# Optimization experiments

Measured on AMD Instinct MI355X. Metric: run time of the kernel, lower is better.

## Reference

```python
import jax, jax.numpy as jnp
import numpy as np

NUM_GROUPS = 32
NUM_HEADS = 8
EPS = 1e-5


def setup_inputs() -> dict:
    key = jax.random.key(0)
    ks = jax.random.split(key, 4)
    b, c, h, w = 16, 512, 32, 32
    x = jax.random.normal(ks[0], (b, c, h, w), dtype=jnp.float32)
    norm_w = jnp.ones((c,), dtype=jnp.float32)
    norm_b = jnp.zeros((c,), dtype=jnp.float32)
    qkv_w = jax.random.normal(ks[1], (3 * c, c), dtype=jnp.float32) * (1.0 / np.sqrt(c))
    qkv_b = jnp.zeros((3 * c,), dtype=jnp.float32)
    proj_w = jax.random.normal(ks[2], (c, c), dtype=jnp.float32) * (1.0 / np.sqrt(c))
    proj_b = jnp.zeros((c,), dtype=jnp.float32)
    return {"x": x, "norm_w": norm_w, "norm_b": norm_b,
            "qkv_w": qkv_w, "qkv_b": qkv_b, "proj_w": proj_w, "proj_b": proj_b}


def group_norm(x, weight, bias):
    b, c, h, w = x.shape
    xg = x.reshape(b, NUM_GROUPS, c // NUM_GROUPS, h * w)
    mean = xg.mean(axis=(2, 3), keepdims=True)
    var = xg.var(axis=(2, 3), keepdims=True)
    xn = (xg - mean) * jax.lax.rsqrt(var + EPS)
    xn = xn.reshape(b, c, h, w)
    return xn * weight[None, :, None, None] + bias[None, :, None, None]


def reference(x, norm_w, norm_b, qkv_w, qkv_b, proj_w, proj_b):
    b, c, h, w = x.shape
    n = h * w
    head = NUM_HEADS
    ch = c // head

    x_norm = group_norm(x, norm_w, norm_b)
    # 1x1 conv == channel matmul: [b,3c,n]
    xf = x_norm.reshape(b, c, n)
    qkv = jnp.einsum('oc,bcn->bon', qkv_w, xf) + qkv_b[None, :, None]
    q, k, v = jnp.split(qkv, 3, axis=1)  # each [b,c,n]
    q = q.reshape(b, head, ch, n) * (ch ** -0.5)
    k = k.reshape(b, head, ch, n)
    v = v.reshape(b, head, ch, n)

    attn = jnp.einsum('bhcn,bhcm->bhnm', q, k)
    attn = jax.nn.softmax(attn, axis=-1)
    out = jnp.einsum('bhnm,bhcm->bhcn', attn, v)  # [b,head,ch,n]
    out = out.reshape(b, c, n)
    out = jnp.einsum('oc,bcn->bon', proj_w, out) + proj_b[None, :, None]
    return x + out.reshape(b, c, h, w)
```

## Files before the change

### kernel.cpp

```cpp
#include <hip/hip_runtime.h>

typedef short short8 __attribute__((ext_vector_type(8)));
typedef short short4v __attribute__((ext_vector_type(4)));
typedef float f32x4 __attribute__((ext_vector_type(4)));

#define B_   16
#define C_   512
#define N_   1024
#define NH_  8
#define CH_  64
#define G_   32
#define CPG_ 16

#if __has_builtin(__builtin_amdgcn_mfma_f32_16x16x16bf16_1k)
#define HAVE_M16 1
#endif

__device__ inline float b2f(unsigned int u) {
    union { unsigned int i; float f; } v; v.i = u << 16; return v.f;
}
__device__ inline unsigned short f2b(float f) {
    union { float f; unsigned int i; } v; v.f = f;
    unsigned int r = v.i + 0x7fffu + ((v.i >> 16) & 1u);
    return (unsigned short)(r >> 16);
}
__device__ inline unsigned int pack2(float a, float b) {
    return (unsigned int)f2b(a) | ((unsigned int)f2b(b) << 16);
}
__device__ inline unsigned int asu(float f) {
    union { float f; unsigned int i; } v; v.f = f; return v.i;
}
__device__ inline unsigned int packtr(float a, float b) {
    return __builtin_amdgcn_perm(asu(b), asu(a), 0x07060302u);
}
__device__ inline void gload16(const void* g, void* l) {
    __builtin_amdgcn_global_load_lds(
        (const __attribute__((address_space(1))) void*)g,
        (__attribute__((address_space(3))) void*)l, 16, 0, 0);
}

__global__ __launch_bounds__(256) void gnconv_kernel(const float* __restrict__ x,
                                                     const float* __restrict__ nw,
                                                     const float* __restrict__ nb,
                                                     unsigned short* __restrict__ xnT,
                                                     const float* __restrict__ qkvw,
                                                     const float* __restrict__ projw,
                                                     unsigned short* __restrict__ wq,
                                                     unsigned short* __restrict__ wp)
{
    __shared__ float red[8];
    int t = threadIdx.x;

    if (blockIdx.x >= 512) {
        const int NQ = 3 * C_ * C_;
        int idx = (((int)blockIdx.x - 512) * 256 + t) * 8;
        const float* src; unsigned short* dst; int j;
        if (idx < NQ) { src = qkvw;  dst = wq; j = idx; }
        else          { src = projw; dst = wp; j = idx - NQ; }
        float4 u0 = *(const float4*)(src + j);
        float4 u1 = *(const float4*)(src + j + 4);
        uint4 p;
        p.x = pack2(u0.x, u0.y); p.y = pack2(u0.z, u0.w);
        p.z = pack2(u1.x, u1.y); p.w = pack2(u1.z, u1.w);
        *(uint4*)(dst + j) = p;
        return;
    }

    int b = blockIdx.x >> 5, g = blockIdx.x & 31;
    const float* base = x + ((size_t)(b * C_ + g * CPG_)) * N_;

    float s = 0.f, ss = 0.f;
    for (int it = 0; it < 16; ++it) {
        int idx = (it * 256 + t) * 4;
        float4 u = *(const float4*)(base + idx);
        s  += u.x + u.y + u.z + u.w;
        ss += u.x * u.x + u.y * u.y + u.z * u.z + u.w * u.w;
    }
#pragma unroll
    for (int off = 1; off < 64; off <<= 1) {
        s  += __shfl_xor(s, off);
        ss += __shfl_xor(ss, off);
    }
    int wv = t >> 6;
    if ((t & 63) == 0) { red[wv * 2] = s; red[wv * 2 + 1] = ss; }
    __syncthreads();
    s  = red[0] + red[2] + red[4] + red[6];
    ss = red[1] + red[3] + red[5] + red[7];
    float mean = s * (1.f / 16384.f);
    float var  = ss * (1.f / 16384.f) - mean * mean;
    float rstd = rsqrtf(var + 1e-5f);

    float sc[16], sh[16];
#pragma unroll
    for (int ch = 0; ch < 16; ++ch) {
        float wv_ = nw[g * CPG_ + ch];
        float bv_ = nb[g * CPG_ + ch];
        sc[ch] = wv_ * rstd;
        sh[ch] = bv_ - mean * sc[ch];
    }

#pragma unroll
    for (int nbi = 0; nbi < 2; ++nbi) {
        int n = nbi * 512 + t * 2;
        float2 v[16];
#pragma unroll
        for (int ch = 0; ch < 16; ++ch)
            v[ch] = *(const float2*)(base + (size_t)ch * N_ + n);
#pragma unroll
        for (int col = 0; col < 2; ++col) {
            float f[16];
#pragma unroll
            for (int ch = 0; ch < 16; ++ch) {
                float xv = col ? v[ch].y : v[ch].x;
                f[ch] = xv * sc[ch] + sh[ch];
            }
            uint4 o0, o1;
            o0.x = pack2(f[0], f[1]);  o0.y = pack2(f[2], f[3]);
            o0.z = pack2(f[4], f[5]);  o0.w = pack2(f[6], f[7]);
            o1.x = pack2(f[8], f[9]);  o1.y = pack2(f[10], f[11]);
            o1.z = pack2(f[12], f[13]); o1.w = pack2(f[14], f[15]);
            unsigned short* dst = xnT + ((size_t)(b * N_ + n + col)) * C_ + g * CPG_;
            *(uint4*)dst = o0;
            *(uint4*)(dst + 8) = o1;
        }
    }
}

__global__ __launch_bounds__(256) void qkv_kernel(const unsigned short* __restrict__ w,
                                                  const float* __restrict__ bias,
                                                  const unsigned short* __restrict__ xnT,
                                                  unsigned short* __restrict__ qT,
                                                  unsigned short* __restrict__ kT,
                                                  unsigned short* __restrict__ vv)
{
    __shared__ unsigned short Als[128 * 64], Bls[128 * 64];
    int t = threadIdx.x;
    int n0 = blockIdx.x * 128, m0 = blockIdx.y * 128, b = blockIdx.z;
    int lane = t & 63, wv = t >> 6;
    int l = lane & 15, qd = lane >> 4;
    int wm = (wv >> 1) * 64, wn = (wv & 1) * 64;
    f32x4 acc[4][4] = {};
    const unsigned short* Bbase = xnT + ((size_t)(b * N_ + n0)) * C_;

    int grow = lane >> 3, gcol = ((lane & 7) ^ grow) * 8;
    const unsigned short* pA[4]; const unsigned short* pB[4];
    unsigned short* lA[4]; unsigned short* lB[4];
#pragma unroll
    for (int g = 0; g < 4; ++g) {
        int r = wv * 32 + g * 8 + grow;
        pA[g] = w + (size_t)(m0 + r) * C_ + gcol;
        pB[g] = Bbase + (size_t)r * C_ + gcol;
        lA[g] = &Als[(wv * 32 + g * 8) * 64];
        lB[g] = &Bls[(wv * 32 + g * 8) * 64];
    }

    for (int kk = 0; kk < 8; ++kk) {
        int ko = kk * 64;
#pragma unroll
        for (int g = 0; g < 4; ++g) {
            gload16(pA[g] + ko, lA[g]);
            gload16(pB[g] + ko, lB[g]);
        }
        __builtin_amdgcn_s_waitcnt(0);
        __syncthreads();
#pragma unroll
        for (int ks = 0; ks < 2; ++ks) {
            short8 aF[4], bF[4];
#pragma unroll
            for (int i = 0; i < 4; ++i) {
                int ra = wm + i * 16 + l;
                aF[i] = *(const short8*)&Als[ra * 64 + (((ks * 4 + qd) ^ (l & 7)) * 8)];
                int rb = wn + i * 16 + l;
                bF[i] = *(const short8*)&Bls[rb * 64 + (((ks * 4 + qd) ^ (l & 7)) * 8)];
            }
#pragma unroll
            for (int mt = 0; mt < 4; ++mt)
#pragma unroll
                for (int nt = 0; nt < 4; ++nt)
                    acc[mt][nt] = __builtin_amdgcn_mfma_f32_16x16x32_bf16(aF[mt], bF[nt], acc[mt][nt], 0, 0, 0);
        }
        __syncthreads();
    }

    int o_base = m0 + wm;
    int sec = o_base >> 9;
    int oc = o_base & 511;
    int h = oc >> 6;
    float bv[4][4];
#pragma unroll
    for (int mt = 0; mt < 4; ++mt)
#pragma unroll
        for (int r = 0; r < 4; ++r)
            bv[mt][r] = bias[o_base + mt * 16 + qd * 4 + r];

    if (sec < 2) {
        unsigned short* dst = (sec == 0) ? qT : kT;
        float scl = (sec == 0) ? (0.125f * 1.44269504f) : 1.0f;
#pragma unroll
        for (int mt = 0; mt < 4; ++mt)
#pragma unroll
            for (int nt = 0; nt < 4; ++nt) {
                int n = n0 + wn + nt * 16 + l;
                ushort4 o;
                o.x = f2b((acc[mt][nt][0] + bv[mt][0]) * scl);
                o.y = f2b((acc[mt][nt][1] + bv[mt][1]) * scl);
                o.z = f2b((acc[mt][nt][2] + bv[mt][2]) * scl);
                o.w = f2b((acc[mt][nt][3] + bv[mt][3]) * scl);
                *(ushort4*)(dst + ((size_t)(b * NH_ + h) * N_ + n) * CH_ + mt * 16 + qd * 4) = o;
            }
    } else {
#pragma unroll
        for (int mt = 0; mt < 4; ++mt)
#pragma unroll
            for (int nt = 0; nt < 4; ++nt) {
                int n = n0 + wn + nt * 16 + l;
#pragma unroll
                for (int r = 0; r < 4; ++r) {
                    int ch = mt * 16 + qd * 4 + r;
                    vv[((size_t)(b * NH_ + h) * CH_ + ch) * N_ + n] = f2b(acc[mt][nt][r] + bv[mt][r]);
                }
            }
    }
}

__global__ __launch_bounds__(256, 4) void attn_kernel(const unsigned short* __restrict__ qT,
                                                      const unsigned short* __restrict__ kT,
                                                      const unsigned short* __restrict__ vv,
                                                      unsigned short* __restrict__ at)
{
    __shared__ unsigned short Ks[2][4096];
    __shared__ unsigned short Vs[2][4096];

    int t = threadIdx.x, lane = t & 63, wv = t >> 6;
    int l = lane & 15, qd = lane >> 4;
    int blk = blockIdx.x;
    int ibk = blk >> 7;
    int bh  = blk & 127;
    int h = bh & 7, b = bh >> 3;
    int i0 = ibk * 128 + wv * 32;
    const size_t hoff = (size_t)bh * (size_t)N_ * CH_;
    const unsigned short* qbase = qT + hoff;
    const unsigned short* kbase = kT + hoff;
    const unsigned short* vbase = vv + hoff;

#ifndef HAVE_M16
    int plok;
    {
        unsigned int ta = (unsigned int)lane, tb = 64u + (unsigned int)lane;
        asm volatile("v_permlane32_swap_b32 %0, %1" : "+v"(ta), "+v"(tb));
        asm volatile("v_permlane16_swap_b32 %0, %1" : "+v"(ta), "+v"(tb));
        unsigned int e1 = (unsigned int)((lane >> 4) * 32 + (lane & 15));
        plok = __all(ta == e1) && __all(tb == e1 + 16u);
    }
    int la0 = (qd & 1) * 32 + l;
    int la1 = la0 + 16;
#endif

    short8 qF[2][2];
#pragma unroll
    for (int it = 0; it < 2; ++it)
#pragma unroll
        for (int ks = 0; ks < 2; ++ks)
            qF[it][ks] = *(const short8*)(qbase + (size_t)(i0 + it * 16 + l) * CH_ + ks * 32 + qd * 8);

    int srow = t >> 2, sc16 = (t & 3) * 16;
    int sw = srow & 7, bb = (t & 3) * 2;
    int d0 = srow * 64 + ((bb ^ sw) * 8);
    int d1 = srow * 64 + (((bb + 1) ^ sw) * 8);
    const unsigned short* kSrc = kbase + (size_t)srow * CH_ + sc16;
    const unsigned short* vSrc = vbase + (size_t)srow * N_ + sc16;

    f32x4 Oa[4][2] = {};
    float lsum[2] = {0.f, 0.f};
    int swl = l & 7;

    uint4 ku0, ku1, vu0, vu1;
    {
        const uint4* kp = (const uint4*)(kSrc);
        ku0 = kp[0]; ku1 = kp[1];
        const uint4* vp2 = (const uint4*)(vSrc);
        vu0 = vp2[0]; vu1 = vp2[1];
        *(uint4*)&Ks[0][d0] = ku0; *(uint4*)&Ks[0][d1] = ku1;
        *(uint4*)&Vs[0][d0] = vu0; *(uint4*)&Vs[0][d1] = vu1;
        kp  = (const uint4*)(kSrc + 4096);
        ku0 = kp[0]; ku1 = kp[1];
        vp2 = (const uint4*)(vSrc + 64);
        vu0 = vp2[0]; vu1 = vp2[1];
    }

    for (int tile = 0; tile < 16; ++tile) {
        __syncthreads();
        if (tile < 15) {
            unsigned short* Kw = Ks[(tile + 1) & 1];
            unsigned short* Vw = Vs[(tile + 1) & 1];
            *(uint4*)&Kw[d0] = ku0; *(uint4*)&Kw[d1] = ku1;
            *(uint4*)&Vw[d0] = vu0; *(uint4*)&Vw[d1] = vu1;
            if (tile < 14) {
                const uint4* kp = (const uint4*)(kSrc + (size_t)(tile + 2) * 4096);
                ku0 = kp[0]; ku1 = kp[1];
                const uint4* vp2 = (const uint4*)(vSrc + (size_t)(tile + 2) * 64);
                vu0 = vp2[0]; vu1 = vp2[1];
            }
        }
        const unsigned short* Kb = Ks[tile & 1];
        const unsigned short* Vb = Vs[tile & 1];
#pragma unroll
        for (int jb = 0; jb < 2; ++jb) {
            short8 kA[2][2];
#pragma unroll
            for (int jt = 0; jt < 2; ++jt)
#pragma unroll
                for (int ks = 0; ks < 2; ++ks)
                    kA[jt][ks] = *(const short8*)&Kb[(jb * 32 + jt * 16 + l) * 64 + (((ks * 4 + qd) ^ swl) * 8)];
            f32x4 Sa[2][2] = {};
#pragma unroll
            for (int jt = 0; jt < 2; ++jt)
#pragma unroll
                for (int it = 0; it < 2; ++it)
#pragma unroll
                    for (int ks = 0; ks < 2; ++ks)
                        Sa[jt][it] = __builtin_amdgcn_mfma_f32_16x16x32_bf16(kA[jt][ks], qF[it][ks], Sa[jt][it], 0, 0, 0);
            unsigned int pk[2][2][2];
#pragma unroll
            for (int jt = 0; jt < 2; ++jt)
#pragma unroll
                for (int it = 0; it < 2; ++it) {
                    float p0 = __builtin_amdgcn_exp2f(Sa[jt][it][0]);
                    float p1 = __builtin_amdgcn_exp2f(Sa[jt][it][1]);
                    float p2 = __builtin_amdgcn_exp2f(Sa[jt][it][2]);
                    float p3 = __builtin_amdgcn_exp2f(Sa[jt][it][3]);
                    lsum[it] += (p0 + p1) + (p2 + p3);
                    pk[jt][it][0] = packtr(p0, p1);
                    pk[jt][it][1] = packtr(p2, p3);
                }
#ifdef HAVE_M16
#pragma unroll
            for (int jt = 0; jt < 2; ++jt) {
                short4v bV[4];
#pragma unroll
                for (int cht = 0; cht < 4; ++cht) {
                    int blkv = jb * 4 + jt * 2 + (qd >> 1);
                    bV[cht] = *(const short4v*)&Vb[(cht * 16 + l) * 64 + ((blkv ^ swl) * 8) + (qd & 1) * 4];
                }
#pragma unroll
                for (int it = 0; it < 2; ++it) {
                    union { unsigned int u[2]; short4v s; } ap;
                    ap.u[0] = pk[jt][it][0]; ap.u[1] = pk[jt][it][1];
#pragma unroll
                    for (int cht = 0; cht < 4; ++cht)
                        Oa[cht][it] = __builtin_amdgcn_mfma_f32_16x16x16bf16_1k(ap.s, bV[cht], Oa[cht][it], 0, 0, 0);
                }
            }
#else
            short8 bP[2];
            if (plok) {
#pragma unroll
                for (int it = 0; it < 2; ++it) {
                    union { short8 s; unsigned int u[4]; } fb;
                    unsigned int a0 = pk[0][it][0], c0 = pk[1][it][0];
                    asm volatile("v_permlane32_swap_b32 %0, %1" : "+v"(a0), "+v"(c0));
                    asm volatile("v_permlane16_swap_b32 %0, %1" : "+v"(a0), "+v"(c0));
                    unsigned int a1 = pk[0][it][1], c1 = pk[1][it][1];
                    asm volatile("v_permlane32_swap_b32 %0, %1" : "+v"(a1), "+v"(c1));
                    asm volatile("v_permlane16_swap_b32 %0, %1" : "+v"(a1), "+v"(c1));
                    fb.u[0] = a0; fb.u[1] = a1; fb.u[2] = c0; fb.u[3] = c1;
                    bP[it] = fb.s;
                }
            } else {
#pragma unroll
                for (int it = 0; it < 2; ++it) {
                    union { short8 s; unsigned int u[4]; } fb;
                    unsigned int a0 = (unsigned int)__shfl((int)pk[0][it][0], la0);
                    unsigned int b0 = (unsigned int)__shfl((int)pk[1][it][0], la0);
                    fb.u[0] = (qd < 2) ? a0 : b0;
                    unsigned int a1 = (unsigned int)__shfl((int)pk[0][it][1], la0);
                    unsigned int b1 = (unsigned int)__shfl((int)pk[1][it][1], la0);
                    fb.u[1] = (qd < 2) ? a1 : b1;
                    unsigned int a2 = (unsigned int)__shfl((int)pk[0][it][0], la1);
                    unsigned int b2 = (unsigned int)__shfl((int)pk[1][it][0], la1);
                    fb.u[2] = (qd < 2) ? a2 : b2;
                    unsigned int a3 = (unsigned int)__shfl((int)pk[0][it][1], la1);
                    unsigned int b3 = (unsigned int)__shfl((int)pk[1][it][1], la1);
                    fb.u[3] = (qd < 2) ? a3 : b3;
                    bP[it] = fb.s;
                }
            }
            short8 vA[4];
#pragma unroll
            for (int cht = 0; cht < 4; ++cht)
                vA[cht] = *(const short8*)&Vb[(cht * 16 + l) * 64 + (((jb * 4 + qd) ^ swl) * 8)];
#pragma unroll
            for (int cht = 0; cht < 4; ++cht)
#pragma unroll
                for (int it = 0; it < 2; ++it)
                    Oa[cht][it] = __builtin_amdgcn_mfma_f32_16x16x32_bf16(vA[cht], bP[it], Oa[cht][it], 0, 0, 0);
#endif
        }
    }

#ifdef HAVE_M16
#pragma unroll
    for (int it = 0; it < 2; ++it) {
        float lt = lsum[it];
        lt += __shfl_xor(lt, 16);
        lt += __shfl_xor(lt, 32);
        float invv[4];
#pragma unroll
        for (int r = 0; r < 4; ++r)
            invv[r] = 1.0f / __shfl(lt, qd * 4 + r);
#pragma unroll
        for (int cht = 0; cht < 4; ++cht)
#pragma unroll
            for (int r = 0; r < 4; ++r) {
                int i = i0 + it * 16 + qd * 4 + r;
                at[((size_t)(b * N_ + i)) * C_ + h * CH_ + cht * 16 + l] = f2b(Oa[cht][it][r] * invv[r]);
            }
    }
#else
#pragma unroll
    for (int it = 0; it < 2; ++it) {
        float lt = lsum[it];
        lt += __shfl_xor(lt, 16);
        lt += __shfl_xor(lt, 32);
        float inv = 1.0f / lt;
        int i = i0 + it * 16 + l;
        unsigned short* dst = at + ((size_t)(b * N_ + i)) * C_ + h * CH_;
#pragma unroll
        for (int cht = 0; cht < 4; ++cht) {
            ushort4 o;
            o.x = f2b(Oa[cht][it][0] * inv);
            o.y = f2b(Oa[cht][it][1] * inv);
            o.z = f2b(Oa[cht][it][2] * inv);
            o.w = f2b(Oa[cht][it][3] * inv);
            *(ushort4*)(dst + cht * 16 + qd * 4) = o;
        }
    }
#endif
}

__global__ __launch_bounds__(256) void proj_kernel(const unsigned short* __restrict__ w,
                                                   const float* __restrict__ bias,
                                                   const unsigned short* __restrict__ at,
                                                   const float* __restrict__ x,
                                                   float* __restrict__ out)
{
    __shared__ unsigned short Als[128 * 64], Bls[128 * 64];
    int t = threadIdx.x;
    int n0 = blockIdx.x * 128, m0 = blockIdx.y * 128, b = blockIdx.z;
    int lane = t & 63, wv = t >> 6;
    int l = lane & 15, qd = lane >> 4;
    int wm = (wv >> 1) * 64, wn = (wv & 1) * 64;
    f32x4 acc[4][4] = {};
    const unsigned short* Bbase = at + ((size_t)(b * N_ + n0)) * C_;

    int grow = lane >> 3, gcol = ((lane & 7) ^ grow) * 8;
    const unsigned short* pA[4]; const unsigned short* pB[4];
    unsigned short* lA[4]; unsigned short* lB[4];
#pragma unroll
    for (int g = 0; g < 4; ++g) {
        int r = wv * 32 + g * 8 + grow;
        pA[g] = w + (size_t)(m0 + r) * C_ + gcol;
        pB[g] = Bbase + (size_t)r * C_ + gcol;
        lA[g] = &Als[(wv * 32 + g * 8) * 64];
        lB[g] = &Bls[(wv * 32 + g * 8) * 64];
    }

    for (int kk = 0; kk < 8; ++kk) {
        int ko = kk * 64;
#pragma unroll
        for (int g = 0; g < 4; ++g) {
            gload16(pA[g] + ko, lA[g]);
            gload16(pB[g] + ko, lB[g]);
        }
        __builtin_amdgcn_s_waitcnt(0);
        __syncthreads();
#pragma unroll
        for (int ks = 0; ks < 2; ++ks) {
            short8 aF[4], bF[4];
#pragma unroll
            for (int i = 0; i < 4; ++i) {
                int ra = wm + i * 16 + l;
                aF[i] = *(const short8*)&Als[ra * 64 + (((ks * 4 + qd) ^ (l & 7)) * 8)];
                int rb = wn + i * 16 + l;
                bF[i] = *(const short8*)&Bls[rb * 64 + (((ks * 4 + qd) ^ (l & 7)) * 8)];
            }
#pragma unroll
            for (int mt = 0; mt < 4; ++mt)
#pragma unroll
                for (int nt = 0; nt < 4; ++nt)
                    acc[mt][nt] = __builtin_amdgcn_mfma_f32_16x16x32_bf16(aF[mt], bF[nt], acc[mt][nt], 0, 0, 0);
        }
        __syncthreads();
    }

    float bv[4][4];
#pragma unroll
    for (int mt = 0; mt < 4; ++mt)
#pragma unroll
        for (int r = 0; r < 4; ++r)
            bv[mt][r] = bias[m0 + wm + mt * 16 + qd * 4 + r];

#pragma unroll
    for (int mt = 0; mt < 4; ++mt)
#pragma unroll
        for (int nt = 0; nt < 4; ++nt) {
            int n = n0 + wn + nt * 16 + l;
#pragma unroll
            for (int r = 0; r < 4; ++r) {
                int o = m0 + wm + mt * 16 + qd * 4 + r;
                size_t idx = ((size_t)b * C_ + o) * N_ + n;
                out[idx] = acc[mt][nt][r] + bv[mt][r] + x[idx];
            }
        }
}

extern "C" void kernel_launch(void* const* d_in, const int* in_sizes, int n_in,
                              void* d_out, int out_size, void* d_ws, size_t ws_size,
                              hipStream_t stream) {
    const float* x     = (const float*)d_in[0];
    const float* nw    = (const float*)d_in[1];
    const float* nb    = (const float*)d_in[2];
    const float* qkvw  = (const float*)d_in[3];
    const float* qkvb  = (const float*)d_in[4];
    const float* projw = (const float*)d_in[5];
    const float* projb = (const float*)d_in[6];
    float* out = (float*)d_out;
    char* ws = (char*)d_ws;
    const size_t SZ = (size_t)B_ * N_ * C_ * 2;
    unsigned short* xnT = (unsigned short*)(ws);
    unsigned short* qTp = (unsigned short*)(ws + SZ);
    unsigned short* kTp = (unsigned short*)(ws + 2 * SZ);
    unsigned short* vp  = (unsigned short*)(ws + 3 * SZ);
    unsigned short* atp = (unsigned short*)(ws);
    unsigned short* wq  = (unsigned short*)(ws + 4 * SZ);
    unsigned short* wp  = (unsigned short*)(ws + 4 * SZ + (size_t)3 * C_ * C_ * 2);

    hipLaunchKernelGGL(gnconv_kernel, dim3(1024), dim3(256), 0, stream, x, nw, nb, xnT, qkvw, projw, wq, wp);
    hipLaunchKernelGGL(qkv_kernel,    dim3(8, 12, B_), dim3(256), 0, stream, wq, qkvb, xnT, qTp, kTp, vp);
    hipLaunchKernelGGL(attn_kernel,   dim3(1024), dim3(256), 0, stream, qTp, kTp, vp, atp);
    hipLaunchKernelGGL(proj_kernel,   dim3(8, 4, B_), dim3(256), 0, stream, wp, projb, atp, x, out);
}
```

Before: 219.7 us.

## Use 16x16x16 MFMA with V as A operand via pre-fragmented padded LDS layout

Removes the compile-time branch between the 16x16x16 MFMA path and the permlane/shuffle 16x16x32 path, always using the 16x16x16 bf16 MFMA with V as the A operand and P as the B operand. V is stored into LDS in a new padded, fragment-ready layout (blocks of 264 shorts) so each lane reads its 4-element fragment with one 8-byte load. The output is then row-oriented, so the epilogue writes vectorized ushort4 stores instead of scalar scattered stores. This trades more but smaller LDS stores and twice as many MFMAs for removing the cross-lane permutes and improving output store coalescing.

```diff
diff --git a/kernel.cpp b/kernel.cpp
--- a/kernel.cpp
+++ b/kernel.cpp
@@ -11,10 +11,6 @@
 #define CH_  64
 #define G_   32
 #define CPG_ 16
-
-#if __has_builtin(__builtin_amdgcn_mfma_f32_16x16x16bf16_1k)
-#define HAVE_M16 1
-#endif
 
 __device__ inline float b2f(unsigned int u) {
     union { unsigned int i; float f; } v; v.i = u << 16; return v.f;
@@ -229,7 +225,7 @@
                                                       unsigned short* __restrict__ at)
 {
     __shared__ unsigned short Ks[2][4096];
-    __shared__ unsigned short Vs[2][4096];
+    __shared__ unsigned short Vs[2][4224];
 
     int t = threadIdx.x, lane = t & 63, wv = t >> 6;
     int l = lane & 15, qd = lane >> 4;
@@ -243,19 +239,6 @@
     const unsigned short* kbase = kT + hoff;
     const unsigned short* vbase = vv + hoff;
 
-#ifndef HAVE_M16
-    int plok;
-    {
-        unsigned int ta = (unsigned int)lane, tb = 64u + (unsigned int)lane;
-        asm volatile("v_permlane32_swap_b32 %0, %1" : "+v"(ta), "+v"(tb));
-        asm volatile("v_permlane16_swap_b32 %0, %1" : "+v"(ta), "+v"(tb));
-        unsigned int e1 = (unsigned int)((lane >> 4) * 32 + (lane & 15));
-        plok = __all(ta == e1) && __all(tb == e1 + 16u);
-    }
-    int la0 = (qd & 1) * 32 + l;
-    int la1 = la0 + 16;
-#endif
-
     short8 qF[2][2];
 #pragma unroll
     for (int it = 0; it < 2; ++it)
@@ -263,12 +246,18 @@
         for (int ks = 0; ks < 2; ++ks)
             qF[it][ks] = *(const short8*)(qbase + (size_t)(i0 + it * 16 + l) * CH_ + ks * 32 + qd * 8);
 
-    int srow = t >> 2, sc16 = (t & 3) * 16;
-    int sw = srow & 7, bb = (t & 3) * 2;
+    int srow = t >> 2, p = t & 3;
+    int sw = srow & 7, bb = p * 2;
     int d0 = srow * 64 + ((bb ^ sw) * 8);
     int d1 = srow * 64 + (((bb + 1) ^ sw) * 8);
-    const unsigned short* kSrc = kbase + (size_t)srow * CH_ + sc16;
-    const unsigned short* vSrc = vbase + (size_t)srow * N_ + sc16;
+    int lch = srow & 15, chtS = srow >> 4;
+    int vblk = p * 4 + chtS;
+    int vd[4];
+#pragma unroll
+    for (int w = 0; w < 4; ++w)
+        vd[w] = vblk * 264 + (w * 16 + lch) * 4;
+    const unsigned short* kSrc = kbase + (size_t)srow * CH_ + p * 16;
+    const unsigned short* vSrc = vbase + (size_t)srow * N_ + p * 16;
 
     f32x4 Oa[4][2] = {};
     float lsum[2] = {0.f, 0.f};
@@ -281,7 +270,10 @@
         const uint4* vp2 = (const uint4*)(vSrc);
         vu0 = vp2[0]; vu1 = vp2[1];
         *(uint4*)&Ks[0][d0] = ku0; *(uint4*)&Ks[0][d1] = ku1;
-        *(uint4*)&Vs[0][d0] = vu0; *(uint4*)&Vs[0][d1] = vu1;
+        *(uint2*)&Vs[0][vd[0]] = make_uint2(vu0.x, vu0.y);
+        *(uint2*)&Vs[0][vd[1]] = make_uint2(vu0.z, vu0.w);
+        *(uint2*)&Vs[0][vd[2]] = make_uint2(vu1.x, vu1.y);
+        *(uint2*)&Vs[0][vd[3]] = make_uint2(vu1.z, vu1.w);
         kp  = (const uint4*)(kSrc + 4096);
         ku0 = kp[0]; ku1 = kp[1];
         vp2 = (const uint4*)(vSrc + 64);
@@ -294,7 +286,10 @@
             unsigned short* Kw = Ks[(tile + 1) & 1];
             unsigned short* Vw = Vs[(tile + 1) & 1];
             *(uint4*)&Kw[d0] = ku0; *(uint4*)&Kw[d1] = ku1;
-            *(uint4*)&Vw[d0] = vu0; *(uint4*)&Vw[d1] = vu1;
+            *(uint2*)&Vw[vd[0]] = make_uint2(vu0.x, vu0.y);
+            *(uint2*)&Vw[vd[1]] = make_uint2(vu0.z, vu0.w);
+            *(uint2*)&Vw[vd[2]] = make_uint2(vu1.x, vu1.y);
+            *(uint2*)&Vw[vd[3]] = make_uint2(vu1.z, vu1.w);
             if (tile < 14) {
                 const uint4* kp = (const uint4*)(kSrc + (size_t)(tile + 2) * 4096);
                 ku0 = kp[0]; ku1 = kp[1];
@@ -333,14 +328,14 @@
                     pk[jt][it][0] = packtr(p0, p1);
                     pk[jt][it][1] = packtr(p2, p3);
                 }
-#ifdef HAVE_M16
 #pragma unroll
             for (int jt = 0; jt < 2; ++jt) {
-                short4v bV[4];
+                short4v vA[4];
 #pragma unroll
                 for (int cht = 0; cht < 4; ++cht) {
-                    int blkv = jb * 4 + jt * 2 + (qd >> 1);
-                    bV[cht] = *(const short4v*)&Vb[(cht * 16 + l) * 64 + ((blkv ^ swl) * 8) + (qd & 1) * 4];
+                    union { uint2 u; short4v s; } vr;
+                    vr.u = *(const uint2*)&Vb[((jb * 2 + jt) * 4 + cht) * 264 + (qd * 16 + l) * 4];
+                    vA[cht] = vr.s;
                 }
 #pragma unroll
                 for (int it = 0; it < 2; ++it) {
@@ -348,75 +343,12 @@
                     ap.u[0] = pk[jt][it][0]; ap.u[1] = pk[jt][it][1];
 #pragma unroll
                     for (int cht = 0; cht < 4; ++cht)
-                        Oa[cht][it] = __builtin_amdgcn_mfma_f32_16x16x16bf16_1k(ap.s, bV[cht], Oa[cht][it], 0, 0, 0);
+                        Oa[cht][it] = __builtin_amdgcn_mfma_f32_16x16x16bf16_1k(vA[cht], ap.s, Oa[cht][it], 0, 0, 0);
                 }
             }
-#else
-            short8 bP[2];
-            if (plok) {
-#pragma unroll
-                for (int it = 0; it < 2; ++it) {
-                    union { short8 s; unsigned int u[4]; } fb;
-                    unsigned int a0 = pk[0][it][0], c0 = pk[1][it][0];
-                    asm volatile("v_permlane32_swap_b32 %0, %1" : "+v"(a0), "+v"(c0));
-                    asm volatile("v_permlane16_swap_b32 %0, %1" : "+v"(a0), "+v"(c0));
-                    unsigned int a1 = pk[0][it][1], c1 = pk[1][it][1];
-                    asm volatile("v_permlane32_swap_b32 %0, %1" : "+v"(a1), "+v"(c1));
-                    asm volatile("v_permlane16_swap_b32 %0, %1" : "+v"(a1), "+v"(c1));
-                    fb.u[0] = a0; fb.u[1] = a1; fb.u[2] = c0; fb.u[3] = c1;
-                    bP[it] = fb.s;
-                }
-            } else {
-#pragma unroll
-                for (int it = 0; it < 2; ++it) {
-                    union { short8 s; unsigned int u[4]; } fb;
-                    unsigned int a0 = (unsigned int)__shfl((int)pk[0][it][0], la0);
-                    unsigned int b0 = (unsigned int)__shfl((int)pk[1][it][0], la0);
-                    fb.u[0] = (qd < 2) ? a0 : b0;
-                    unsigned int a1 = (unsigned int)__shfl((int)pk[0][it][1], la0);
-                    unsigned int b1 = (unsigned int)__shfl((int)pk[1][it][1], la0);
-                    fb.u[1] = (qd < 2) ? a1 : b1;
-                    unsigned int a2 = (unsigned int)__shfl((int)pk[0][it][0], la1);
-                    unsigned int b2 = (unsigned int)__shfl((int)pk[1][it][0], la1);
-                    fb.u[2] = (qd < 2) ? a2 : b2;
-                    unsigned int a3 = (unsigned int)__shfl((int)pk[0][it][1], la1);
-                    unsigned int b3 = (unsigned int)__shfl((int)pk[1][it][1], la1);
-                    fb.u[3] = (qd < 2) ? a3 : b3;
-                    bP[it] = fb.s;
-                }
-            }
-            short8 vA[4];
-#pragma unroll
-            for (int cht = 0; cht < 4; ++cht)
-                vA[cht] = *(const short8*)&Vb[(cht * 16 + l) * 64 + (((jb * 4 + qd) ^ swl) * 8)];
-#pragma unroll
-            for (int cht = 0; cht < 4; ++cht)
-#pragma unroll
-                for (int it = 0; it < 2; ++it)
-                    Oa[cht][it] = __builtin_amdgcn_mfma_f32_16x16x32_bf16(vA[cht], bP[it], Oa[cht][it], 0, 0, 0);
-#endif
-        }
-    }
-
-#ifdef HAVE_M16
-#pragma unroll
-    for (int it = 0; it < 2; ++it) {
-        float lt = lsum[it];
-        lt += __shfl_xor(lt, 16);
-        lt += __shfl_xor(lt, 32);
-        float invv[4];
-#pragma unroll
-        for (int r = 0; r < 4; ++r)
-            invv[r] = 1.0f / __shfl(lt, qd * 4 + r);
-#pragma unroll
-        for (int cht = 0; cht < 4; ++cht)
-#pragma unroll
-            for (int r = 0; r < 4; ++r) {
-                int i = i0 + it * 16 + qd * 4 + r;
-                at[((size_t)(b * N_ + i)) * C_ + h * CH_ + cht * 16 + l] = f2b(Oa[cht][it][r] * invv[r]);
-            }
-    }
-#else
+        }
+    }
+
 #pragma unroll
     for (int it = 0; it < 2; ++it) {
         float lt = lsum[it];
@@ -435,7 +367,6 @@
             *(ushort4*)(dst + cht * 16 + qd * 4) = o;
         }
     }
-#endif
 }
 
 __global__ __launch_bounds__(256) void proj_kernel(const unsigned short* __restrict__ w,
```

After: 212.6 us. 3.2% less time.
